# Kernel tuning notes

Measured on AMD Instinct MI355X. Metric: run time of the kernel, lower is better.

## Reference

```python
import jax, jax.numpy as jnp
import numpy as np

N, E, F_IN, H, C = 50000, 800000, 128, 4, 73
HC = H * C  # 292
NEG_SLOPE_ATT = 0.2   # GATv2 attention leaky relu
NEG_SLOPE_ACT = 0.01  # F.leaky_relu default
BN_EPS = 1e-5


def setup_inputs() -> dict:
    key = jax.random.key(0)
    ks = jax.random.split(key, 20)
    rn = lambda k, shp, s=0.05: (jax.random.normal(k, shp, jnp.float32) * s)
    inp = {
        'x': jax.random.normal(ks[0], (N, F_IN), jnp.float32),
        'edge_index': jax.random.randint(ks[1], (2, E), 0, N, jnp.int64),
        # conv1 (in=F_IN)
        'Wl1': rn(ks[2], (HC, F_IN)), 'bl1': rn(ks[3], (HC,)),
        'Wr1': rn(ks[4], (HC, F_IN)), 'br1': rn(ks[5], (HC,)),
        'att1': rn(ks[6], (H, C)), 'b1': rn(ks[7], (HC,)),
        # conv2 (in=HC)
        'Wl2': rn(ks[8], (HC, HC)), 'bl2': rn(ks[9], (HC,)),
        'Wr2': rn(ks[10], (HC, HC)), 'br2': rn(ks[11], (HC,)),
        'att2': rn(ks[12], (H, C)), 'b2': rn(ks[13], (HC,)),
        # shared BatchNorm1d(HC)
        'gamma': jnp.ones((HC,), jnp.float32), 'beta': jnp.zeros((HC,), jnp.float32),
        # classifier Linear(HC, 2)
        'Wc': rn(ks[14], (2, HC)), 'bc': rn(ks[15], (2,)),
    }
    return inp


def _gatv2(x, src, dst, Wl, bl, Wr, br, att, b):
    # lin_l on source, lin_r on target (PyG GATv2Conv, share_weights=False)
    xl = (x @ Wl.T + bl).reshape(-1, H, C)  # [N,H,C]
    xr = (x @ Wr.T + br).reshape(-1, H, C)
    f = xl[src] + xr[dst]                    # [E,H,C] edge-wise gather
    s = jnp.einsum('ehc,hc->eh', jax.nn.leaky_relu(f, NEG_SLOPE_ATT), att)
    # segment softmax over incoming edges of each destination node
    m = jax.ops.segment_max(s, dst, num_segments=N)
    ex = jnp.exp(s - m[dst])
    den = jax.ops.segment_sum(ex, dst, num_segments=N)
    alpha = ex / (den[dst] + 1e-16)          # [E,H]
    out = jax.ops.segment_sum(alpha[:, :, None] * xl[src], dst, num_segments=N)
    return out.reshape(-1, HC) + b           # concat heads + bias


def _bn(x, gamma, beta):
    mu = jnp.mean(x, axis=0)
    var = jnp.mean((x - mu) ** 2, axis=0)
    return (x - mu) * jax.lax.rsqrt(var + BN_EPS) * gamma + beta


def reference(x, edge_index, Wl1, bl1, Wr1, br1, att1, b1,
              Wl2, bl2, Wr2, br2, att2, b2, gamma, beta, Wc, bc):
    src, dst = edge_index[0], edge_index[1]
    h = _gatv2(x, src, dst, Wl1, bl1, Wr1, br1, att1, b1)
    h = jax.nn.leaky_relu(_bn(h, gamma, beta), NEG_SLOPE_ACT)
    h = _gatv2(h, src, dst, Wl2, bl2, Wr2, br2, att2, b2)
    h = jax.nn.leaky_relu(_bn(h, gamma, beta), NEG_SLOPE_ACT)
    return h @ Wc.T + bc
```

## Files before the change

kernel.cpp:

```cpp
#include <hip/hip_runtime.h>

#define HCDIM 292
#define NHEAD 4
#define CDIM 73
#define SLOTS 5
#define NPERM 320
#define BN_EPS 1e-5f
#define LOG2E 1.44269504f

using u16x8 = __attribute__((ext_vector_type(8))) unsigned short;
using f32x4 = __attribute__((ext_vector_type(4))) float;
using u16x4 = __attribute__((ext_vector_type(4))) unsigned short;
using hf2   = __attribute__((ext_vector_type(2))) _Float16;
using v2h   = __attribute__((ext_vector_type(2))) __fp16;
using v8h   = __attribute__((ext_vector_type(8))) __fp16;

__device__ inline v2h pkrtz(float a, float b) {
  return __builtin_amdgcn_cvt_pkrtz(a, b);
}
__device__ inline float fdot2(hf2 a, hf2 b, float c) {
  return __builtin_amdgcn_fdot2(__builtin_bit_cast(v2h, a),
                                __builtin_bit_cast(v2h, b), c, false);
}
__device__ inline ushort f2h(float f) {
  _Float16 h = (_Float16)f;
  return __builtin_bit_cast(ushort, h);
}
__device__ inline float h2f(ushort v) {
  return (float)__builtin_bit_cast(_Float16, v);
}
__device__ inline hf2 habs2(hf2 a) {
  unsigned u = __builtin_bit_cast(unsigned, a) & 0x7fff7fffu;
  return __builtin_bit_cast(hf2, u);
}

__device__ inline int perm2feat(int p, bool& valid) {
  int h, c;
  if (p < 256) {
    h = p >> 6;
    c = ((p & 3) << 4) | ((p >> 2) & 15);
    valid = true;
  } else {
    int q = p - 256;
    h = q >> 4;
    c = 64 + (q & 15);
    valid = (q & 15) < (CDIM - 64);
  }
  return h * CDIM + c;
}

__global__ void k_wperm(const float* __restrict__ W, const float* __restrict__ b,
                        ushort* __restrict__ Wp, float* __restrict__ pb,
                        int Kin, int Kpad, int kperm) {
  int p = blockIdx.x, t = threadIdx.x;
  bool pv;
  int gn = perm2feat(p, pv);
  int gk = t;
  bool kv = t < Kin;
  if (kperm) { bool v2; gk = perm2feat(t, v2); kv = v2; }
  ushort v = 0;
  if (pv && kv) v = f2h(W[(size_t)gn * Kin + gk]);
  Wp[(size_t)p * Kpad + t] = v;
  if (t == 0) pb[p] = pv ? b[gn] : 0.f;
}

__global__ void k_vecperm(const float* __restrict__ att1, const float* __restrict__ b1,
                          const float* __restrict__ att2, const float* __restrict__ b2,
                          const float* __restrict__ gamma, const float* __restrict__ beta,
                          const float* __restrict__ Wc, float* __restrict__ o) {
  int p = threadIdx.x, w = blockIdx.x;
  bool pv;
  int gn = perm2feat(p, pv);
  const float* src;
  switch (w) {
    case 0: src = att1; break;
    case 1: src = b1; break;
    case 2: src = att2; break;
    case 3: src = b2; break;
    case 4: src = gamma; break;
    case 5: src = beta; break;
    case 6: src = Wc; break;
    default: src = Wc + HCDIM; break;
  }
  o[w * NPERM + p] = pv ? src[gn] : 0.f;
}

__global__ void k_hist(const int* __restrict__ dst, int* __restrict__ deg, int E) {
  int i = blockIdx.x * blockDim.x + threadIdx.x;
  if (i < E) atomicAdd(&deg[dst[i]], 1);
}

__global__ __launch_bounds__(256) void k_block_sum(const int* __restrict__ deg,
                                                   int* __restrict__ bsum, int n) {
  __shared__ int s[256];
  int i = blockIdx.x * 256 + threadIdx.x;
  s[threadIdx.x] = (i < n) ? deg[i] : 0;
  __syncthreads();
  for (int off = 128; off > 0; off >>= 1) {
    if (threadIdx.x < off) s[threadIdx.x] += s[threadIdx.x + off];
    __syncthreads();
  }
  if (threadIdx.x == 0) bsum[blockIdx.x] = s[0];
}

__global__ __launch_bounds__(256) void k_scan_small(const int* __restrict__ bsum,
                                                    int* __restrict__ boff, int G) {
  __shared__ int s[256];
  int t = threadIdx.x;
  int v = (t < G) ? bsum[t] : 0;
  s[t] = v;
  __syncthreads();
  for (int off = 1; off < 256; off <<= 1) {
    int tv = (t >= off) ? s[t - off] : 0;
    __syncthreads();
    s[t] += tv;
    __syncthreads();
  }
  if (t < G) boff[t] = s[t] - v;
}

__global__ __launch_bounds__(256) void k_scan_final(const int* __restrict__ deg,
                                                    const int* __restrict__ boff,
                                                    int* __restrict__ row_ptr,
                                                    int* __restrict__ cursor,
                                                    int n, int E) {
  __shared__ int s[256];
  int t = threadIdx.x;
  int i = blockIdx.x * 256 + t;
  int v = (i < n) ? deg[i] : 0;
  s[t] = v;
  __syncthreads();
  for (int off = 1; off < 256; off <<= 1) {
    int tv = (t >= off) ? s[t - off] : 0;
    __syncthreads();
    s[t] += tv;
    __syncthreads();
  }
  if (i < n) {
    int rp = boff[blockIdx.x] + s[t] - v;
    row_ptr[i] = rp;
    cursor[i] = rp;
  }
  if (i == 0) row_ptr[n] = E;
}

__global__ void k_csr_fill(const int* __restrict__ srcs, const int* __restrict__ dsts,
                           int* __restrict__ cursor, int* __restrict__ csr_src, int E) {
  int i = blockIdx.x * blockDim.x + threadIdx.x;
  if (i < E) {
    int pos = atomicAdd(&cursor[dsts[i]], 1);
    csr_src[pos] = srcs[i];
  }
}

template <bool CVT>
__device__ inline void load_af(const char* const (&Ar)[4], int koff, int quad,
                               v8h (&af)[4]) {
#pragma unroll
  for (int i = 0; i < 4; ++i) {
    if (CVT) {
      const float* p = (const float*)Ar[i] + koff + quad * 8;
      float4 f0 = *(const float4*)p;
      float4 f1 = *(const float4*)(p + 4);
      union { v2h h[4]; v8h v; } u;
      u.h[0] = pkrtz(f0.x, f0.y);
      u.h[1] = pkrtz(f0.z, f0.w);
      u.h[2] = pkrtz(f1.x, f1.y);
      u.h[3] = pkrtz(f1.z, f1.w);
      af[i] = u.v;
    } else {
      af[i] = *(const v8h*)((const ushort*)Ar[i] + koff + quad * 8);
    }
  }
}

template <int KS, bool CVT>
__global__ __launch_bounds__(256) void k_gemm_blds(
    const void* __restrict__ Av, const ushort* __restrict__ Wb,
    const float* __restrict__ pb, ushort* __restrict__ o0,
    ushort* __restrict__ o1, int M, int miters) {
  constexpr int KSTEPS = KS / 32;
  constexpr int BSTR = KS + 8;
  __shared__ ushort Bs[80 * BSTR];
  int b = blockIdx.x;
  int mlo = b & 7, ct = (b >> 3) & 7, mhi = b >> 6;
  int mc = mlo + 8 * mhi;
  ushort* out = (ct < 4) ? o0 : o1;
  const int colbase = (ct & 3) * 80;
  const int tid = threadIdx.x;
  const int wave = tid >> 6, lane = tid & 63;
  const int quad = lane >> 4, lr = lane & 15;
  const int esz = CVT ? 4 : 2;

  for (int idx = tid; idx < 80 * (KS / 8); idx += 256) {
    int r = idx / (KS / 8), c8 = idx - r * (KS / 8);
    *(u16x8*)(Bs + r * BSTR + c8 * 8) =
        *(const u16x8*)(Wb + (size_t)(ct * 80 + r) * KS + c8 * 8);
  }
  __syncthreads();

  const ushort* bp[5];
#pragma unroll
  for (int i = 0; i < 5; ++i) bp[i] = Bs + (i * 16 + lr) * BSTR;

  float4 pbv[5];
#pragma unroll
  for (int ni = 0; ni < 5; ++ni)
    pbv[ni] = *(const float4*)(pb + ct * 80 + ni * 16 + quad * 4);

  for (int it = mc; it < miters; it += 64) {
    int mbase = it * 256 + wave * 64;
    const char* Ar[4];
#pragma unroll
    for (int i = 0; i < 4; ++i) {
      int ar = mbase + i * 16 + lr;
      if (ar >= M) ar = M - 1;
      Ar[i] = (const char*)Av + (size_t)ar * KS * esz;
    }
    f32x4 acc[4][5] = {};
    v8h afb[2][4];
    load_af<CVT>(Ar, 0, quad, afb[0]);
#pragma unroll
    for (int s = 0; s < KSTEPS; ++s) {
      if (s + 1 < KSTEPS) load_af<CVT>(Ar, (s + 1) * 32, quad, afb[(s + 1) & 1]);
      v8h bf[5];
#pragma unroll
      for (int i = 0; i < 5; ++i)
        bf[i] = *(const v8h*)(bp[i] + s * 32 + quad * 8);
#pragma unroll
      for (int ni = 0; ni < 5; ++ni)
#pragma unroll
        for (int mi = 0; mi < 4; ++mi)
          acc[mi][ni] = __builtin_amdgcn_mfma_f32_16x16x32_f16(
              bf[ni], afb[s & 1][mi], acc[mi][ni], 0, 0, 0);
    }
#pragma unroll
    for (int mi = 0; mi < 4; ++mi) {
      int gm = mbase + mi * 16 + lr;
      if (gm >= M) continue;
      ushort* orow = out + (size_t)gm * NPERM + colbase + quad * 4;
#pragma unroll
      for (int ni = 0; ni < 5; ++ni) {
        union { v2h h[2]; u16x4 o; } u;
        u.h[0] = pkrtz(acc[mi][ni][0] + pbv[ni].x, acc[mi][ni][1] + pbv[ni].y);
        u.h[1] = pkrtz(acc[mi][ni][2] + pbv[ni].z, acc[mi][ni][3] + pbv[ni].w);
        *(u16x4*)(orow + ni * 16) = u.o;
      }
    }
  }
}

__global__ __launch_bounds__(256) void k_pre(const ushort* __restrict__ xl,
                                             const float* __restrict__ attp,
                                             float* __restrict__ pl, int n) {
  int wave = threadIdx.x >> 6, lane = threadIdx.x & 63;
  int d = blockIdx.x * 4 + wave;
  if (d >= n) return;
  int hgrp = lane >> 4, li = lane & 15;
  const float C = 0.4f * LOG2E;
  float4 a4 = *(const float4*)(attp + lane * 4);
  hf2 av01{(_Float16)(C * a4.x), (_Float16)(C * a4.y)};
  hf2 av23{(_Float16)(C * a4.z), (_Float16)(C * a4.w)};
  hf2 av5{(_Float16)(C * attp[256 + lane]), (_Float16)0.f};

  uint2 cc = *(const uint2*)(xl + (size_t)d * NPERM + lane * 4);
  ushort c5 = xl[(size_t)d * NPERM + 256 + lane];
  hf2 c01 = __builtin_bit_cast(hf2, cc.x);
  hf2 c23 = __builtin_bit_cast(hf2, cc.y);
  hf2 c5h{__builtin_bit_cast(_Float16, c5), (_Float16)0.f};

  float Ta = fdot2(c01, av01, fdot2(c23, av23, fdot2(c5h, av5, 0.f)));
#pragma unroll
  for (int off = 1; off < 16; off <<= 1) Ta += __shfl_xor(Ta, off, 64);
  if (li == 0) pl[d * 4 + hgrp] = 1.5f * Ta;
}

__global__ __launch_bounds__(256) void k_agg(const ushort* __restrict__ xl,
                                             const ushort* __restrict__ xr,
                                             const float* __restrict__ pl,
                                             const int* __restrict__ csr_src,
                                             const int* __restrict__ row_ptr,
                                             const float* __restrict__ attp,
                                             const float* __restrict__ bp,
                                             ushort* __restrict__ out, int n) {
  int wave = threadIdx.x >> 6, lane = threadIdx.x & 63;
  int d = blockIdx.x * 4 + wave;
  if (d >= n) return;
  int hgrp = lane >> 4;
  int start = __builtin_amdgcn_readfirstlane(row_ptr[d]);
  int end = __builtin_amdgcn_readfirstlane(row_ptr[d + 1]);

  float4 bp4 = *(const float4*)(bp + lane * 4);
  float bp5 = bp[256 + lane];

  if (start >= end) {
    union { v2h h[2]; u16x4 o; } u;
    u.h[0] = pkrtz(bp4.x, bp4.y);
    u.h[1] = pkrtz(bp4.z, bp4.w);
    *(u16x4*)(out + (size_t)d * NPERM + lane * 4) = u.o;
    out[(size_t)d * NPERM + 256 + lane] = f2h(bp5);
    return;
  }

  const float C = 0.4f * LOG2E;
  float4 at4 = *(const float4*)(attp + lane * 4);
  hf2 av01{(_Float16)(C * at4.x), (_Float16)(C * at4.y)};
  hf2 av23{(_Float16)(C * at4.z), (_Float16)(C * at4.w)};
  hf2 av5{(_Float16)(C * attp[256 + lane]), (_Float16)0.f};

  hf2 xr01, xr23, xr5;
  {
    uint2 rr = *(const uint2*)(xr + (size_t)d * NPERM + lane * 4);
    xr01 = __builtin_bit_cast(hf2, rr.x);
    xr23 = __builtin_bit_cast(hf2, rr.y);
    xr5 = hf2{__builtin_bit_cast(_Float16, xr[(size_t)d * NPERM + 256 + lane]),
              (_Float16)0.f};
  }
  float Tb = fdot2(xr01, av01, fdot2(xr23, av23, fdot2(xr5, av5, 0.f)));
  Tb += __shfl_xor(Tb, 1, 64);
  Tb += __shfl_xor(Tb, 2, 64);
  Tb += __shfl_xor(Tb, 4, 64);
  Tb += __shfl_xor(Tb, 8, 64);
  float prv = 1.5f * Tb;
  float acc[SLOTS] = {};
  float den = 0.f;
  int dg = end - start;
  int nfull = dg >> 2;
  int rem = dg & 3;

  uint2 s8[4];
  ushort s1[4];
  float sp[4];
#pragma unroll
  for (int k = 0; k < 4; ++k) {
    int e = start + k;
    if (e > end - 1) e = end - 1;
    int s = __builtin_amdgcn_readfirstlane(csr_src[e]);
    s8[k] = *(const uint2*)(xl + (size_t)s * NPERM + lane * 4);
    s1[k] = xl[(size_t)s * NPERM + 256 + lane];
    sp[k] = pl[s * 4 + hgrp];
  }

  for (int g = 0; g < nfull; ++g) {
    int ebase = start + g * 4 + 4;
    uint2 n8[4];
    ushort n1[4];
    float np[4];
#pragma unroll
    for (int k = 0; k < 4; ++k) {
      int e = ebase + k;
      if (e > end - 1) e = end - 1;
      int s = __builtin_amdgcn_readfirstlane(csr_src[e]);
      n8[k] = *(const uint2*)(xl + (size_t)s * NPERM + lane * 4);
      n1[k] = xl[(size_t)s * NPERM + 256 + lane];
      np[k] = pl[s * 4 + hgrp];
    }

    hf2 x01[4], x23[4], x5[4];
    float T[4];
#pragma unroll
    for (int k = 0; k < 4; ++k) {
      x01[k] = __builtin_bit_cast(hf2, s8[k].x);
      x23[k] = __builtin_bit_cast(hf2, s8[k].y);
      x5[k] = hf2{__builtin_bit_cast(_Float16, s1[k]), (_Float16)0.f};
      T[k] = fdot2(habs2(x01[k] + xr01), av01,
             fdot2(habs2(x23[k] + xr23), av23,
             fdot2(habs2(x5[k] + xr5), av5, 0.f)));
    }
#pragma unroll
    for (int off = 1; off <= 8; off <<= 1) {
#pragma unroll
      for (int k = 0; k < 4; ++k) T[k] += __shfl_xor(T[k], off, 64);
    }
    float w[4];
#pragma unroll
    for (int k = 0; k < 4; ++k) {
      w[k] = exp2f(fminf(T[k] + sp[k] + prv, 80.f));
      den += w[k];
    }
#pragma unroll
    for (int k = 0; k < 4; ++k) {
      acc[0] = fmaf(w[k], (float)x01[k][0], acc[0]);
      acc[1] = fmaf(w[k], (float)x01[k][1], acc[1]);
      acc[2] = fmaf(w[k], (float)x23[k][0], acc[2]);
      acc[3] = fmaf(w[k], (float)x23[k][1], acc[3]);
      acc[4] = fmaf(w[k], (float)x5[k][0], acc[4]);
    }
#pragma unroll
    for (int k = 0; k < 4; ++k) { s8[k] = n8[k]; s1[k] = n1[k]; sp[k] = np[k]; }
  }

#pragma unroll
  for (int k = 0; k < 3; ++k) {
    if (k < rem) {
      hf2 x01 = __builtin_bit_cast(hf2, s8[k].x);
      hf2 x23 = __builtin_bit_cast(hf2, s8[k].y);
      hf2 x5{__builtin_bit_cast(_Float16, s1[k]), (_Float16)0.f};
      float T = fdot2(habs2(x01 + xr01), av01,
                fdot2(habs2(x23 + xr23), av23,
                fdot2(habs2(x5 + xr5), av5, 0.f)));
      T += __shfl_xor(T, 1, 64);
      T += __shfl_xor(T, 2, 64);
      T += __shfl_xor(T, 4, 64);
      T += __shfl_xor(T, 8, 64);
      float w = exp2f(fminf(T + sp[k] + prv, 80.f));
      den += w;
      acc[0] = fmaf(w, (float)x01[0], acc[0]);
      acc[1] = fmaf(w, (float)x01[1], acc[1]);
      acc[2] = fmaf(w, (float)x23[0], acc[2]);
      acc[3] = fmaf(w, (float)x23[1], acc[3]);
      acc[4] = fmaf(w, (float)x5[0], acc[4]);
    }
  }

  float inv = 1.f / (den + 1e-16f);
  union { v2h h[2]; u16x4 o; } u;
  u.h[0] = pkrtz(fmaf(acc[0], inv, bp4.x), fmaf(acc[1], inv, bp4.y));
  u.h[1] = pkrtz(fmaf(acc[2], inv, bp4.z), fmaf(acc[3], inv, bp4.w));
  *(u16x4*)(out + (size_t)d * NPERM + lane * 4) = u.o;
  out[(size_t)d * NPERM + 256 + lane] = f2h(fmaf(acc[4], inv, bp5));
}

__global__ __launch_bounds__(320) void k_bn_reduce(const ushort* __restrict__ h,
                                                   float* __restrict__ colsum,
                                                   float* __restrict__ colsq,
                                                   int n, int rows_per_block) {
  int c = threadIdx.x;
  int r0 = blockIdx.x * rows_per_block;
  int r1 = min(r0 + rows_per_block, n);
  float s = 0.f, s2 = 0.f;
  for (int r = r0; r < r1; ++r) {
    float v = h2f(h[(size_t)r * NPERM + c]);
    s += v;
    s2 += v * v;
  }
  atomicAdd(&colsum[c], s);
  atomicAdd(&colsq[c], s2);
}

__global__ void k_bn_coef(float* __restrict__ colsum, float* __restrict__ colsq,
                          const float* __restrict__ gp, const float* __restrict__ bp,
                          float invN) {
  int c = threadIdx.x + blockIdx.x * blockDim.x;
  if (c >= NPERM) return;
  float mu = colsum[c] * invN;
  float var = colsq[c] * invN - mu * mu;
  float scale = rsqrtf(var + BN_EPS) * gp[c];
  colsum[c] = scale;
  colsq[c] = bp[c] - mu * scale;
}

__global__ void k_bn_apply_bf(const ushort* __restrict__ h,
                              const float* __restrict__ scale,
                              const float* __restrict__ shift,
                              ushort* __restrict__ outb, int total8) {
  int i = blockIdx.x * blockDim.x + threadIdx.x;
  if (i >= total8) return;
  int cg = i - (i / 40) * 40;
  u16x8 v = *(const u16x8*)(h + (size_t)i * 8);
  float f[8];
#pragma unroll
  for (int k = 0; k < 8; ++k) {
    int c = cg * 8 + k;
    float t = fmaf(h2f(v[k]), scale[c], shift[c]);
    f[k] = (t > 0.f) ? t : 0.01f * t;
  }
  union { v2h h4[4]; u16x8 o; } u;
#pragma unroll
  for (int k = 0; k < 4; ++k)
    u.h4[k] = pkrtz(f[2 * k], f[2 * k + 1]);
  *(u16x8*)(outb + (size_t)i * 8) = u.o;
}

__global__ __launch_bounds__(256) void k_bn_classifier(
    const ushort* __restrict__ h, const float* __restrict__ scale,
    const float* __restrict__ shift, const float* __restrict__ wc0,
    const float* __restrict__ wc1, const float* __restrict__ bc,
    float* __restrict__ out, int n) {
  int wave = threadIdx.x >> 6, lane = threadIdx.x & 63;
  int r = blockIdx.x * 4 + wave;
  if (r >= n) return;
  float a0 = 0.f, a1 = 0.f;
#pragma unroll
  for (int k = 0; k < SLOTS; ++k) {
    int slot = lane + 64 * k;
    float v = fmaf(h2f(h[(size_t)r * NPERM + slot]), scale[slot], shift[slot]);
    v = (v > 0.f) ? v : 0.01f * v;
    a0 = fmaf(v, wc0[slot], a0);
    a1 = fmaf(v, wc1[slot], a1);
  }
#pragma unroll
  for (int off = 32; off > 0; off >>= 1) {
    a0 += __shfl_xor(a0, off, 64);
    a1 += __shfl_xor(a1, off, 64);
  }
  if (lane == 0) {
    out[(size_t)2 * r] = a0 + bc[0];
    out[(size_t)2 * r + 1] = a1 + bc[1];
  }
}

extern "C" void kernel_launch(void* const* d_in, const int* in_sizes, int n_in,
                              void* d_out, int out_size, void* d_ws, size_t ws_size,
                              hipStream_t stream) {
  const float* x      = (const float*)d_in[0];
  const int*   eidx   = (const int*)d_in[1];
  const float* Wl1    = (const float*)d_in[2];
  const float* bl1    = (const float*)d_in[3];
  const float* Wr1    = (const float*)d_in[4];
  const float* br1    = (const float*)d_in[5];
  const float* att1   = (const float*)d_in[6];
  const float* b1     = (const float*)d_in[7];
  const float* Wl2    = (const float*)d_in[8];
  const float* bl2    = (const float*)d_in[9];
  const float* Wr2    = (const float*)d_in[10];
  const float* br2    = (const float*)d_in[11];
  const float* att2   = (const float*)d_in[12];
  const float* b2     = (const float*)d_in[13];
  const float* gamma  = (const float*)d_in[14];
  const float* beta   = (const float*)d_in[15];
  const float* Wc     = (const float*)d_in[16];
  const float* bc     = (const float*)d_in[17];
  float* out = (float*)d_out;

  const int FIN = 128;
  const int N = in_sizes[0] / FIN;
  const int E = in_sizes[1] / 2;

  const int* src = eidx;
  const int* dst = eidx + E;

  ushort* h      = (ushort*)d_ws;
  ushort* xl     = h + (size_t)N * NPERM;
  ushort* xr     = xl + (size_t)N * NPERM;
  ushort* abuf   = xr + (size_t)N * NPERM;
  ushort* wb     = abuf + (size_t)N * NPERM;
  float* pb      = (float*)(wb + (size_t)2 * NPERM * NPERM);
  float* vecp    = pb + 2 * NPERM;
  float* pl      = vecp + 8 * NPERM;
  float* colsum  = pl + (size_t)N * NHEAD;
  float* colsq   = colsum + NPERM;
  int* deg       = (int*)(colsq + NPERM);
  int* row_ptr   = deg + N;
  int* cursor    = row_ptr + N + 1;
  int* bsum      = cursor + N;
  int* boff      = bsum + 256;
  int* csr_src   = boff + 256;

  const int G = (N + 255) / 256;
  const int EB = (E + 255) / 256;
  const int AGGB = (N + 3) / 4;
  const int MITERS = (N + 255) / 256;
  const int GEMMB = 512;

  const float* att1p = vecp;
  const float* b1p   = vecp + NPERM;
  const float* att2p = vecp + 2 * NPERM;
  const float* b2p   = vecp + 3 * NPERM;
  const float* gp    = vecp + 4 * NPERM;
  const float* btp   = vecp + 5 * NPERM;
  const float* wc0   = vecp + 6 * NPERM;
  const float* wc1   = vecp + 7 * NPERM;

  hipMemsetAsync(deg, 0, (size_t)N * sizeof(int), stream);
  k_hist<<<EB, 256, 0, stream>>>(dst, deg, E);
  k_block_sum<<<G, 256, 0, stream>>>(deg, bsum, N);
  k_scan_small<<<1, 256, 0, stream>>>(bsum, boff, G);
  k_scan_final<<<G, 256, 0, stream>>>(deg, boff, row_ptr, cursor, N, E);
  k_csr_fill<<<EB, 256, 0, stream>>>(src, dst, cursor, csr_src, E);

  k_vecperm<<<8, NPERM, 0, stream>>>(att1, b1, att2, b2, gamma, beta, Wc, vecp);

  k_wperm<<<NPERM, FIN, 0, stream>>>(Wl1, bl1, wb, pb, FIN, FIN, 0);
  k_wperm<<<NPERM, FIN, 0, stream>>>(Wr1, br1, wb + (size_t)NPERM * FIN, pb + NPERM,
                                     FIN, FIN, 0);
  k_gemm_blds<FIN, true><<<GEMMB, 256, 0, stream>>>((const void*)x, wb, pb,
                                                    xl, xr, N, MITERS);
  k_pre<<<AGGB, 256, 0, stream>>>(xl, att1p, pl, N);
  k_agg<<<AGGB, 256, 0, stream>>>(xl, xr, pl, csr_src, row_ptr, att1p, b1p, h, N);

  const int RPB = (N + 255) / 256;
  hipMemsetAsync(colsum, 0, 2 * NPERM * sizeof(float), stream);
  k_bn_reduce<<<256, NPERM, 0, stream>>>(h, colsum, colsq, N, RPB);
  k_bn_coef<<<2, 160, 0, stream>>>(colsum, colsq, gp, btp, 1.f / (float)N);
  k_bn_apply_bf<<<(N * 40 + 255) / 256, 256, 0, stream>>>(h, colsum, colsq, abuf,
                                                          N * 40);

  k_wperm<<<NPERM, NPERM, 0, stream>>>(Wl2, bl2, wb, pb, HCDIM, NPERM, 1);
  k_wperm<<<NPERM, NPERM, 0, stream>>>(Wr2, br2, wb + (size_t)NPERM * NPERM,
                                       pb + NPERM, HCDIM, NPERM, 1);
  k_gemm_blds<NPERM, false><<<GEMMB, 256, 0, stream>>>((const void*)abuf, wb, pb,
                                                       xl, xr, N, MITERS);
  k_pre<<<AGGB, 256, 0, stream>>>(xl, att2p, pl, N);
  k_agg<<<AGGB, 256, 0, stream>>>(xl, xr, pl, csr_src, row_ptr, att2p, b2p, h, N);

  hipMemsetAsync(colsum, 0, 2 * NPERM * sizeof(float), stream);
  k_bn_reduce<<<256, NPERM, 0, stream>>>(h, colsum, colsq, N, RPB);
  k_bn_coef<<<2, 160, 0, stream>>>(colsum, colsq, gp, btp, 1.f / (float)N);

  k_bn_classifier<<<AGGB, 256, 0, stream>>>(h, colsum, colsq, wc0, wc1, bc, out, N);
}
```

Baseline: 625.7 us.

## Merge weight prep kernels, fuse BN coef into reduce, deepen GEMM A prefetch

All weight, bias and vector permutation kernels are merged into one k_prep launch at the start, with separate buffers for the layer-1 and layer-2 weights. The BN coefficient kernel is folded into k_bn_reduce: the last block to finish, detected through an atomic ticket counter, computes scale and shift. The second GEMM now prefetches A fragments three k-steps ahead instead of one. Together these cut the number of kernel launches and try to hide A-load latency, at the cost of more registers in the K=320 GEMM and a fence-and-atomic handoff at the end of the reduce.

```diff
diff --git a/kernel.cpp b/kernel.cpp
--- a/kernel.cpp
+++ b/kernel.cpp
@@ -5,6 +5,7 @@
 #define CDIM 73
 #define SLOTS 5
 #define NPERM 320
+#define FIN 128
 #define BN_EPS 1e-5f
 #define LOG2E 1.44269504f
 
@@ -49,40 +50,59 @@
   return h * CDIM + c;
 }
 
-__global__ void k_wperm(const float* __restrict__ W, const float* __restrict__ b,
-                        ushort* __restrict__ Wp, float* __restrict__ pb,
-                        int Kin, int Kpad, int kperm) {
-  int p = blockIdx.x, t = threadIdx.x;
-  bool pv;
-  int gn = perm2feat(p, pv);
-  int gk = t;
-  bool kv = t < Kin;
-  if (kperm) { bool v2; gk = perm2feat(t, v2); kv = v2; }
-  ushort v = 0;
-  if (pv && kv) v = f2h(W[(size_t)gn * Kin + gk]);
-  Wp[(size_t)p * Kpad + t] = v;
-  if (t == 0) pb[p] = pv ? b[gn] : 0.f;
-}
-
-__global__ void k_vecperm(const float* __restrict__ att1, const float* __restrict__ b1,
-                          const float* __restrict__ att2, const float* __restrict__ b2,
-                          const float* __restrict__ gamma, const float* __restrict__ beta,
-                          const float* __restrict__ Wc, float* __restrict__ o) {
-  int p = threadIdx.x, w = blockIdx.x;
-  bool pv;
-  int gn = perm2feat(p, pv);
-  const float* src;
-  switch (w) {
-    case 0: src = att1; break;
-    case 1: src = b1; break;
-    case 2: src = att2; break;
-    case 3: src = b2; break;
-    case 4: src = gamma; break;
-    case 5: src = beta; break;
-    case 6: src = Wc; break;
-    default: src = Wc + HCDIM; break;
-  }
-  o[w * NPERM + p] = pv ? src[gn] : 0.f;
+__global__ __launch_bounds__(320) void k_prep(
+    const float* __restrict__ Wl1, const float* __restrict__ bl1,
+    const float* __restrict__ Wr1, const float* __restrict__ br1,
+    const float* __restrict__ Wl2, const float* __restrict__ bl2,
+    const float* __restrict__ Wr2, const float* __restrict__ br2,
+    const float* __restrict__ att1, const float* __restrict__ b1,
+    const float* __restrict__ att2, const float* __restrict__ b2,
+    const float* __restrict__ gamma, const float* __restrict__ beta,
+    const float* __restrict__ Wc, ushort* __restrict__ wb1,
+    float* __restrict__ pb1, ushort* __restrict__ wb2, float* __restrict__ pb2,
+    float* __restrict__ vecp) {
+  int b = blockIdx.x, t = threadIdx.x;
+  if (b < 8) {
+    bool pv;
+    int gn = perm2feat(t, pv);
+    const float* src;
+    switch (b) {
+      case 0: src = att1; break;
+      case 1: src = b1; break;
+      case 2: src = att2; break;
+      case 3: src = b2; break;
+      case 4: src = gamma; break;
+      case 5: src = beta; break;
+      case 6: src = Wc; break;
+      default: src = Wc + HCDIM; break;
+    }
+    vecp[b * NPERM + t] = pv ? src[gn] : 0.f;
+    return;
+  }
+  if (b < 648) {
+    int bb = b - 8;
+    int half = bb / 320, p = bb - half * 320;
+    const float* W = half ? Wr1 : Wl1;
+    const float* bi = half ? br1 : bl1;
+    ushort* Wp = wb1 + (size_t)(half * NPERM + p) * FIN;
+    bool pv;
+    int gn = perm2feat(p, pv);
+    if (t < FIN) Wp[t] = pv ? f2h(W[(size_t)gn * FIN + t]) : (ushort)0;
+    if (t == 0) pb1[half * NPERM + p] = pv ? bi[gn] : 0.f;
+    return;
+  }
+  {
+    int bb = b - 648;
+    int half = bb / 320, p = bb - half * 320;
+    const float* W = half ? Wr2 : Wl2;
+    const float* bi = half ? br2 : bl2;
+    ushort* Wp = wb2 + (size_t)(half * NPERM + p) * NPERM;
+    bool pv, kv;
+    int gn = perm2feat(p, pv);
+    int gk = perm2feat(t, kv);
+    Wp[t] = (pv && kv) ? f2h(W[(size_t)gn * HCDIM + gk]) : (ushort)0;
+    if (t == 0) pb2[half * NPERM + p] = pv ? bi[gn] : 0.f;
+  }
 }
 
 __global__ void k_hist(const int* __restrict__ dst, int* __restrict__ deg, int E) {
@@ -180,6 +200,7 @@
     const float* __restrict__ pb, ushort* __restrict__ o0,
     ushort* __restrict__ o1, int M, int miters) {
   constexpr int KSTEPS = KS / 32;
+  constexpr int AD = CVT ? 2 : 4;
   constexpr int BSTR = KS + 8;
   __shared__ ushort Bs[80 * BSTR];
   int b = blockIdx.x;
@@ -218,11 +239,14 @@
       Ar[i] = (const char*)Av + (size_t)ar * KS * esz;
     }
     f32x4 acc[4][5] = {};
-    v8h afb[2][4];
-    load_af<CVT>(Ar, 0, quad, afb[0]);
+    v8h afb[AD][4];
+#pragma unroll
+    for (int k = 0; k < AD - 1; ++k)
+      if (k < KSTEPS) load_af<CVT>(Ar, k * 32, quad, afb[k % AD]);
 #pragma unroll
     for (int s = 0; s < KSTEPS; ++s) {
-      if (s + 1 < KSTEPS) load_af<CVT>(Ar, (s + 1) * 32, quad, afb[(s + 1) & 1]);
+      if (s + AD - 1 < KSTEPS)
+        load_af<CVT>(Ar, (s + AD - 1) * 32, quad, afb[(s + AD - 1) % AD]);
       v8h bf[5];
 #pragma unroll
       for (int i = 0; i < 5; ++i)
@@ -232,7 +256,7 @@
 #pragma unroll
         for (int mi = 0; mi < 4; ++mi)
           acc[mi][ni] = __builtin_amdgcn_mfma_f32_16x16x32_f16(
-              bf[ni], afb[s & 1][mi], acc[mi][ni], 0, 0, 0);
+              bf[ni], afb[s % AD][mi], acc[mi][ni], 0, 0, 0);
     }
 #pragma unroll
     for (int mi = 0; mi < 4; ++mi) {
@@ -424,7 +448,11 @@
 __global__ __launch_bounds__(320) void k_bn_reduce(const ushort* __restrict__ h,
                                                    float* __restrict__ colsum,
                                                    float* __restrict__ colsq,
-                                                   int n, int rows_per_block) {
+                                                   const float* __restrict__ gp,
+                                                   const float* __restrict__ bp,
+                                                   int* __restrict__ tick,
+                                                   int n, int rows_per_block,
+                                                   float invN, int nblocks) {
   int c = threadIdx.x;
   int r0 = blockIdx.x * rows_per_block;
   int r1 = min(r0 + rows_per_block, n);
@@ -436,18 +464,19 @@
   }
   atomicAdd(&colsum[c], s);
   atomicAdd(&colsq[c], s2);
-}
-
-__global__ void k_bn_coef(float* __restrict__ colsum, float* __restrict__ colsq,
-                          const float* __restrict__ gp, const float* __restrict__ bp,
-                          float invN) {
-  int c = threadIdx.x + blockIdx.x * blockDim.x;
-  if (c >= NPERM) return;
-  float mu = colsum[c] * invN;
-  float var = colsq[c] * invN - mu * mu;
-  float scale = rsqrtf(var + BN_EPS) * gp[c];
-  colsum[c] = scale;
-  colsq[c] = bp[c] - mu * scale;
+  __threadfence();
+  __syncthreads();
+  __shared__ int lastf;
+  if (c == 0) lastf = (atomicAdd(tick, 1) == nblocks - 1) ? 1 : 0;
+  __syncthreads();
+  if (lastf) {
+    __threadfence();
+    float mu = colsum[c] * invN;
+    float var = colsq[c] * invN - mu * mu;
+    float scale = rsqrtf(var + BN_EPS) * gp[c];
+    colsum[c] = scale;
+    colsq[c] = bp[c] - mu * scale;
+  }
 }
 
 __global__ void k_bn_apply_bf(const ushort* __restrict__ h,
@@ -523,7 +552,6 @@
   const float* bc     = (const float*)d_in[17];
   float* out = (float*)d_out;
 
-  const int FIN = 128;
   const int N = in_sizes[0] / FIN;
   const int E = in_sizes[1] / 2;
 
@@ -534,13 +562,16 @@
   ushort* xl     = h + (size_t)N * NPERM;
   ushort* xr     = xl + (size_t)N * NPERM;
   ushort* abuf   = xr + (size_t)N * NPERM;
-  ushort* wb     = abuf + (size_t)N * NPERM;
-  float* pb      = (float*)(wb + (size_t)2 * NPERM * NPERM);
-  float* vecp    = pb + 2 * NPERM;
+  ushort* wb1    = abuf + (size_t)N * NPERM;
+  ushort* wb2    = wb1 + (size_t)2 * NPERM * FIN;
+  float* pb1     = (float*)(wb2 + (size_t)2 * NPERM * NPERM);
+  float* pb2     = pb1 + 2 * NPERM;
+  float* vecp    = pb2 + 2 * NPERM;
   float* pl      = vecp + 8 * NPERM;
   float* colsum  = pl + (size_t)N * NHEAD;
   float* colsq   = colsum + NPERM;
-  int* deg       = (int*)(colsq + NPERM);
+  int* tick      = (int*)(colsq + NPERM);
+  int* deg       = tick + 4;
   int* row_ptr   = deg + N;
   int* cursor    = row_ptr + N + 1;
   int* bsum      = cursor + N;
@@ -562,6 +593,10 @@
   const float* wc0   = vecp + 6 * NPERM;
   const float* wc1   = vecp + 7 * NPERM;
 
+  k_prep<<<1288, 320, 0, stream>>>(Wl1, bl1, Wr1, br1, Wl2, bl2, Wr2, br2,
+                                   att1, b1, att2, b2, gamma, beta, Wc,
+                                   wb1, pb1, wb2, pb2, vecp);
+
   hipMemsetAsync(deg, 0, (size_t)N * sizeof(int), stream);
   k_hist<<<EB, 256, 0, stream>>>(dst, deg, E);
   k_block_sum<<<G, 256, 0, stream>>>(deg, bsum, N);
@@ -569,34 +604,26 @@
   k_scan_final<<<G, 256, 0, stream>>>(deg, boff, row_ptr, cursor, N, E);
   k_csr_fill<<<EB, 256, 0, stream>>>(src, dst, cursor, csr_src, E);
 
-  k_vecperm<<<8, NPERM, 0, stream>>>(att1, b1, att2, b2, gamma, beta, Wc, vecp);
-
-  k_wperm<<<NPERM, FIN, 0, stream>>>(Wl1, bl1, wb, pb, FIN, FIN, 0);
-  k_wperm<<<NPERM, FIN, 0, stream>>>(Wr1, br1, wb + (size_t)NPERM * FIN, pb + NPERM,
-                                     FIN, FIN, 0);
-  k_gemm_blds<FIN, true><<<GEMMB, 256, 0, stream>>>((const void*)x, wb, pb,
+  k_gemm_blds<FIN, true><<<GEMMB, 256, 0, stream>>>((const void*)x, wb1, pb1,
                                                     xl, xr, N, MITERS);
   k_pre<<<AGGB, 256, 0, stream>>>(xl, att1p, pl, N);
   k_agg<<<AGGB, 256, 0, stream>>>(xl, xr, pl, csr_src, row_ptr, att1p, b1p, h, N);
 
   const int RPB = (N + 255) / 256;
-  hipMemsetAsync(colsum, 0, 2 * NPERM * sizeof(float), stream);
-  k_bn_reduce<<<256, NPERM, 0, stream>>>(h, colsum, colsq, N, RPB);
-  k_bn_coef<<<2, 160, 0, stream>>>(colsum, colsq, gp, btp, 1.f / (float)N);
+  hipMemsetAsync(colsum, 0, 2 * NPERM * sizeof(float) + 4 * sizeof(int), stream);
+  k_bn_reduce<<<256, NPERM, 0, stream>>>(h, colsum, colsq, gp, btp, tick, N, RPB,
+                                         1.f / (float)N, 256);
   k_bn_apply_bf<<<(N * 40 + 255) / 256, 256, 0, stream>>>(h, colsum, colsq, abuf,
                                                           N * 40);
 
-  k_wperm<<<NPERM, NPERM, 0, stream>>>(Wl2, bl2, wb, pb, HCDIM, NPERM, 1);
-  k_wperm<<<NPERM, NPERM, 0, stream>>>(Wr2, br2, wb + (size_t)NPERM * NPERM,
-                                       pb + NPERM, HCDIM, NPERM, 1);
-  k_gemm_blds<NPERM, false><<<GEMMB, 256, 0, stream>>>((const void*)abuf, wb, pb,
+  k_gemm_blds<NPERM, false><<<GEMMB, 256, 0, stream>>>((const void*)abuf, wb2, pb2,
                                                        xl, xr, N, MITERS);
   k_pre<<<AGGB, 256, 0, stream>>>(xl, att2p, pl, N);
   k_agg<<<AGGB, 256, 0, stream>>>(xl, xr, pl, csr_src, row_ptr, att2p, b2p, h, N);
 
-  hipMemsetAsync(colsum, 0, 2 * NPERM * sizeof(float), stream);
-  k_bn_reduce<<<256, NPERM, 0, stream>>>(h, colsum, colsq, N, RPB);
-  k_bn_coef<<<2, 160, 0, stream>>>(colsum, colsq, gp, btp, 1.f / (float)N);
+  hipMemsetAsync(colsum, 0, 2 * NPERM * sizeof(float) + 4 * sizeof(int), stream);
+  k_bn_reduce<<<256, NPERM, 0, stream>>>(h, colsum, colsq, gp, btp, tick, N, RPB,
+                                         1.f / (float)N, 256);
 
   k_bn_classifier<<<AGGB, 256, 0, stream>>>(h, colsum, colsq, wc0, wc1, bc, out, N);
 }
```

New measurement: 651.6 us. 1.04x slower.
